# Kernel tuning notes

Hardware: AMD Instinct MI355X
Metric: run time of the kernel (lower is better)

Reference implementation:

```python
import jax, jax.numpy as jnp
import numpy as np

IN_F = 8192
OUT_F = 8192
BATCH = 32


def setup_inputs() -> dict:
    key = jax.random.key(0)
    k_x, k_w, k_s = jax.random.split(key, 3)
    x = jax.random.normal(k_x, (BATCH, IN_F), dtype=jnp.float32)
    # int8-valued weights (stored as int32 for portability), range [-128, 127)
    int8_weights = jax.random.randint(k_w, (IN_F, OUT_F), -128, 127, dtype=jnp.int32)
    scaler = jax.random.uniform(k_s, (1,), dtype=jnp.float32)
    return {"x": x, "int8_weights": int8_weights, "scaler": scaler}


def reference(x, int8_weights, scaler):
    # Dequantize the full weight tensor (as the torch module does), then dense matmul.
    fp_weights = int8_weights.astype(jnp.float32) * scaler  # [in, out]
    return jnp.matmul(x, fp_weights)  # [batch, out]
```

## Files before the change

### kernel.cpp

```cpp
#include <hip/hip_runtime.h>


#define IN_F   8192
#define OUT_F  8192
#define BATCH  32
#define KSPLIT 32
#define KCHUNK (IN_F / KSPLIT)

__global__ void prep_x_kernel(const float* __restrict__ x,
                              const float* __restrict__ scaler,
                              float* __restrict__ xt) {
    int i = blockIdx.x * 256 + threadIdx.x;
    int k = i >> 5;
    int b = i & 31;
    xt[i] = x[b * IN_F + k] * scaler[0];
}

__global__ __launch_bounds__(256, 4)
void lq_main_kernel(const int* __restrict__ w,
                    const float* __restrict__ xt,
                    float* __restrict__ part) {
    __shared__ float4 xs[KCHUNK * (BATCH / 4)];
    const int tid = threadIdx.x;
    const int col = blockIdx.x * 256 + tid;
    const int kc  = blockIdx.y;
    const int k0  = kc * KCHUNK;

    const float4* xg = (const float4*)(xt + (size_t)k0 * BATCH);
#pragma unroll
    for (int j = 0; j < (KCHUNK * BATCH / 4) / 256; ++j)
        xs[j * 256 + tid] = xg[j * 256 + tid];
    __syncthreads();

    float acc[BATCH];
#pragma unroll
    for (int b = 0; b < BATCH; ++b) acc[b] = 0.0f;

    const int* wp = w + (size_t)k0 * OUT_F + col;

#pragma unroll 8
    for (int k = 0; k < KCHUNK; ++k) {
        float wv = (float)wp[(size_t)k * OUT_F];
        const float4* xk = &xs[k * (BATCH / 4)];
#pragma unroll
        for (int q = 0; q < BATCH / 4; ++q) {
            float4 xv = xk[q];
            acc[4 * q + 0] = fmaf(xv.x, wv, acc[4 * q + 0]);
            acc[4 * q + 1] = fmaf(xv.y, wv, acc[4 * q + 1]);
            acc[4 * q + 2] = fmaf(xv.z, wv, acc[4 * q + 2]);
            acc[4 * q + 3] = fmaf(xv.w, wv, acc[4 * q + 3]);
        }
    }

    float* pp = part + (size_t)kc * (BATCH * OUT_F) + col;
#pragma unroll
    for (int b = 0; b < BATCH; ++b)
        pp[(size_t)b * OUT_F] = acc[b];
}

__global__ void reduce_kernel(const float* __restrict__ part,
                              float* __restrict__ out) {
    int i = blockIdx.x * 256 + threadIdx.x;
    float s = 0.0f;
#pragma unroll
    for (int c = 0; c < KSPLIT; ++c)
        s += part[(size_t)c * (BATCH * OUT_F) + i];
    out[i] = s;
}

extern "C" void kernel_launch(void* const* d_in, const int* in_sizes, int n_in,
                              void* d_out, int out_size, void* d_ws, size_t ws_size,
                              hipStream_t stream) {
    const float* x = (const float*)d_in[0];
    const int*   w = (const int*)d_in[1];
    const float* s = (const float*)d_in[2];
    float* out  = (float*)d_out;
    float* xt   = (float*)d_ws;
    float* part = (float*)d_ws + (size_t)BATCH * IN_F;

    prep_x_kernel<<<dim3((BATCH * IN_F) / 256), dim3(256), 0, stream>>>(x, s, xt);

    lq_main_kernel<<<dim3(OUT_F / 256, KSPLIT), dim3(256), 0, stream>>>(w, xt, part);

    reduce_kernel<<<dim3((BATCH * OUT_F) / 256), dim3(256), 0, stream>>>(part, out);
}
```

Measured before the change: 378.8 us.

## Register-block four columns per thread, double K split, vectorize reduction

Each thread now computes four output columns, 256 apart, so every float4 of x read from shared memory feeds four times as many FMAs. This cuts LDS traffic per FMA, which is likely the main bottleneck. To keep enough blocks in flight, KSPLIT grows from 32 to 64 and launch bounds drop to 2 blocks per SM to leave room for 128 accumulators. The cost is a partial-sum buffer twice as large in global memory. The reduce kernel now uses float4 loads to handle that extra traffic.

```diff
diff --git a/kernel.cpp b/kernel.cpp
--- a/kernel.cpp
+++ b/kernel.cpp
@@ -4,8 +4,9 @@
 #define IN_F   8192
 #define OUT_F  8192
 #define BATCH  32
-#define KSPLIT 32
+#define KSPLIT 64
 #define KCHUNK (IN_F / KSPLIT)
+#define CPT    4
 
 __global__ void prep_x_kernel(const float* __restrict__ x,
                               const float* __restrict__ scaler,
@@ -16,13 +17,13 @@
     xt[i] = x[b * IN_F + k] * scaler[0];
 }
 
-__global__ __launch_bounds__(256, 4)
+__global__ __launch_bounds__(256, 2)
 void lq_main_kernel(const int* __restrict__ w,
                     const float* __restrict__ xt,
                     float* __restrict__ part) {
     __shared__ float4 xs[KCHUNK * (BATCH / 4)];
     const int tid = threadIdx.x;
-    const int col = blockIdx.x * 256 + tid;
+    const int colbase = blockIdx.x * (256 * CPT) + tid;
     const int kc  = blockIdx.y;
     const int k0  = kc * KCHUNK;
 
@@ -32,40 +33,53 @@
         xs[j * 256 + tid] = xg[j * 256 + tid];
     __syncthreads();
 
-    float acc[BATCH];
+    float acc[CPT][BATCH];
 #pragma unroll
-    for (int b = 0; b < BATCH; ++b) acc[b] = 0.0f;
+    for (int c = 0; c < CPT; ++c)
+#pragma unroll
+        for (int b = 0; b < BATCH; ++b) acc[c][b] = 0.0f;
 
-    const int* wp = w + (size_t)k0 * OUT_F + col;
+    const int* wp = w + (size_t)k0 * OUT_F + colbase;
 
-#pragma unroll 8
+#pragma unroll 4
     for (int k = 0; k < KCHUNK; ++k) {
-        float wv = (float)wp[(size_t)k * OUT_F];
+        float wv[CPT];
+#pragma unroll
+        for (int c = 0; c < CPT; ++c)
+            wv[c] = (float)wp[(size_t)k * OUT_F + c * 256];
         const float4* xk = &xs[k * (BATCH / 4)];
 #pragma unroll
         for (int q = 0; q < BATCH / 4; ++q) {
             float4 xv = xk[q];
-            acc[4 * q + 0] = fmaf(xv.x, wv, acc[4 * q + 0]);
-            acc[4 * q + 1] = fmaf(xv.y, wv, acc[4 * q + 1]);
-            acc[4 * q + 2] = fmaf(xv.z, wv, acc[4 * q + 2]);
-            acc[4 * q + 3] = fmaf(xv.w, wv, acc[4 * q + 3]);
+#pragma unroll
+            for (int c = 0; c < CPT; ++c) {
+                acc[c][4 * q + 0] = fmaf(xv.x, wv[c], acc[c][4 * q + 0]);
+                acc[c][4 * q + 1] = fmaf(xv.y, wv[c], acc[c][4 * q + 1]);
+                acc[c][4 * q + 2] = fmaf(xv.z, wv[c], acc[c][4 * q + 2]);
+                acc[c][4 * q + 3] = fmaf(xv.w, wv[c], acc[c][4 * q + 3]);
+            }
         }
     }
 
-    float* pp = part + (size_t)kc * (BATCH * OUT_F) + col;
+    float* pp = part + (size_t)kc * (BATCH * OUT_F) + colbase;
 #pragma unroll
     for (int b = 0; b < BATCH; ++b)
-        pp[(size_t)b * OUT_F] = acc[b];
+#pragma unroll
+        for (int c = 0; c < CPT; ++c)
+            pp[(size_t)b * OUT_F + c * 256] = acc[c][b];
 }
 
 __global__ void reduce_kernel(const float* __restrict__ part,
                               float* __restrict__ out) {
     int i = blockIdx.x * 256 + threadIdx.x;
-    float s = 0.0f;
+    float4 s = {0.f, 0.f, 0.f, 0.f};
+    const float4* p4 = (const float4*)part;
 #pragma unroll
-    for (int c = 0; c < KSPLIT; ++c)
-        s += part[(size_t)c * (BATCH * OUT_F) + i];
-    out[i] = s;
+    for (int c = 0; c < KSPLIT; ++c) {
+        float4 v = p4[(size_t)c * (BATCH * OUT_F / 4) + i];
+        s.x += v.x; s.y += v.y; s.z += v.z; s.w += v.w;
+    }
+    ((float4*)out)[i] = s;
 }
 
 extern "C" void kernel_launch(void* const* d_in, const int* in_sizes, int n_in,
@@ -80,7 +94,7 @@
 
     prep_x_kernel<<<dim3((BATCH * IN_F) / 256), dim3(256), 0, stream>>>(x, s, xt);
 
-    lq_main_kernel<<<dim3(OUT_F / 256, KSPLIT), dim3(256), 0, stream>>>(w, xt, part);
+    lq_main_kernel<<<dim3(OUT_F / (256 * CPT), KSPLIT), dim3(256), 0, stream>>>(w, xt, part);
 
-    reduce_kernel<<<dim3((BATCH * OUT_F) / 256), dim3(256), 0, stream>>>(part, out);
+    reduce_kernel<<<dim3((BATCH * OUT_F / 4) / 256), dim3(256), 0, stream>>>(part, out);
 }
```

After: 400.5 us. +5.7%, slower.
